# Performance work log

Hardware: AMD Instinct MI355X
Metric: run time of the kernel (lower is better)

## Reference

```python
import jax, jax.numpy as jnp
import numpy as np

HIDDEN_DIM = 1024
SEQ_LEN = 4096
D_IN = 1024


def setup_inputs() -> dict:
    key = jax.random.key(0)
    ks = jax.random.split(key, 9)
    s = 1.0 / np.sqrt(D_IN)
    return {
        "q": jax.random.normal(ks[0], (SEQ_LEN, D_IN), jnp.float32),
        "k": jax.random.normal(ks[1], (SEQ_LEN, D_IN), jnp.float32),
        "v": jax.random.normal(ks[2], (SEQ_LEN, D_IN), jnp.float32),
        "Wq": jax.random.normal(ks[3], (D_IN, HIDDEN_DIM), jnp.float32) * s,
        "bq": jnp.zeros((HIDDEN_DIM,), jnp.float32),
        "Wk": jax.random.normal(ks[4], (D_IN, HIDDEN_DIM), jnp.float32) * s,
        "bk": jnp.zeros((HIDDEN_DIM,), jnp.float32),
        "Wv": jax.random.normal(ks[5], (D_IN, HIDDEN_DIM), jnp.float32) * s,
        "bv": jnpp_zeros() if False else jnp.zeros((HIDDEN_DIM,), jnp.float32),
    }


def reference(q, k, v, Wq, bq, Wk, bk, Wv, bv):
    # Dense projections (flax Dense: x @ W + b)
    query = q @ Wq + bq          # [S, H]
    key_p = k @ Wk + bk          # [S, H]
    value = v @ Wv + bv          # [S, H]
    # scores = Q K^T / sqrt(hidden_dim)  -> [S, S]
    scores = jnp.matmul(query, key_p.T) / jnp.sqrt(jnp.float32(HIDDEN_DIM))
    weights = jax.nn.softmax(scores, axis=-1)
    context = jnp.matmul(weights, value)  # [S, H]
    return context
```

## Files before the change

### kernel.cpp

```cpp
#include <hip/hip_runtime.h>


typedef short short4v __attribute__((ext_vector_type(4)));
typedef short short8  __attribute__((ext_vector_type(8)));
typedef float f32x4   __attribute__((ext_vector_type(4)));

#define MFMA16 __builtin_amdgcn_mfma_f32_16x16x32_bf16

__device__ __forceinline__ short f2bf(float f) {
    union { float f; unsigned u; } x; x.f = f;
    unsigned r = (x.u + 0x7FFFu + ((x.u >> 16) & 1u)) >> 16;
    return (short)r;
}
__device__ __forceinline__ float bf2f(short s) {
    union { unsigned u; float f; } x;
    x.u = ((unsigned)(unsigned short)s) << 16; return x.f;
}
__device__ __forceinline__ void store_out(short* p, float v) { *p = f2bf(v); }
__device__ __forceinline__ void store_out(float* p, float v) { *p = v; }

__device__ __forceinline__ void gl2lds(const short* g, short* l) {
    __builtin_amdgcn_global_load_lds(
        (const __attribute__((address_space(1))) void*)g,
        (__attribute__((address_space(3))) void*)l, 16, 0, 0);
}

__global__ __launch_bounds__(256) void prep_w(
    const float* __restrict__ W0, const float* __restrict__ W1,
    const float* __restrict__ W2, short* __restrict__ Wt)
{
    __shared__ float tile[64][65];
    const float* W = blockIdx.z == 0 ? W0 : (blockIdx.z == 1 ? W1 : W2);
    short* T = Wt + (size_t)blockIdx.z * 1048576;
    const int c0 = blockIdx.x * 64;
    const int r0 = blockIdx.y * 64;
    const int tx = threadIdx.x & 63;
    const int ty = threadIdx.x >> 6;
    #pragma unroll
    for (int p = 0; p < 16; ++p) {
        int r = ty + p * 4;
        tile[r][tx] = W[(size_t)(r0 + r) * 1024 + c0 + tx];
    }
    __syncthreads();
    #pragma unroll
    for (int p = 0; p < 16; ++p) {
        int r = ty + p * 4;
        T[(size_t)(c0 + r) * 1024 + r0 + tx] = f2bf(tile[tx][r]);
    }
}

__global__ __launch_bounds__(256) void cast_qkv(
    const float* __restrict__ q, const float* __restrict__ k,
    const float* __restrict__ v, short* __restrict__ xb)
{
    const float* src = blockIdx.z == 0 ? q : (blockIdx.z == 1 ? k : v);
    short* dst = xb + (size_t)blockIdx.z * 4194304;
    for (int i = blockIdx.x * 256 + threadIdx.x; i < 1048576; i += 256 * 1024) {
        float4 f = ((const float4*)src)[i];
        short4v o;
        o[0] = f2bf(f.x); o[1] = f2bf(f.y); o[2] = f2bf(f.z); o[3] = f2bf(f.w);
        ((short4v*)dst)[i] = o;
    }
}

__global__ __launch_bounds__(256) void transpose_v(
    const short* __restrict__ src, short* __restrict__ dst)
{
    __shared__ short t[64][65];
    const int c0 = blockIdx.x * 64;
    const int r0 = blockIdx.y * 64;
    const int tx = threadIdx.x & 63;
    const int ty = threadIdx.x >> 6;
    #pragma unroll
    for (int p = 0; p < 16; ++p) {
        const int r = p * 4 + ty;
        t[r][tx] = src[(size_t)(r0 + r) * 1024 + c0 + tx];
    }
    __syncthreads();
    #pragma unroll
    for (int p = 0; p < 16; ++p) {
        const int r = p * 4 + ty;
        dst[(size_t)(c0 + r) * 4096 + r0 + tx] = t[tx][r];
    }
}

template <typename TOut, int MODE>
__global__ __launch_bounds__(512, 2) void gemm256(
    const short* __restrict__ A, const short* __restrict__ Bt,
    const float* __restrict__ b0, const float* __restrict__ b1,
    const float* __restrict__ b2,
    TOut* __restrict__ C, float* __restrict__ P1, float* __restrict__ P2,
    float* __restrict__ P3,
    int M, int N, int lda, int ldb, float scale,
    int nc, int nc_last, int kstep)
{
    __shared__ short Lds[65536];

    const int t    = threadIdx.x;
    const int lane = t & 63;
    const int wv   = t >> 6;

    int m0, n0;
    {
        const int nb  = gridDim.x;
        const int bid = blockIdx.y * nb + blockIdx.x;
        if (nb == 16 && gridDim.y == 16) {
            const int x = bid & 7, i = bid >> 3;
            m0 = ((x & 1) * 8 + (i & 7)) * 256;
            n0 = ((x >> 1) * 4 + (i >> 3)) * 256;
        } else {
            const int band   = bid / (8 * nb);
            const int within = bid - band * 8 * nb;
            m0 = (band * 8 + (within & 7)) * 256;
            n0 = (within >> 3) * 256;
        }
    }

    const float* bias = nullptr;
    int kbeg = 0;
    TOut* Cw = C;
    if constexpr (MODE == 1) {
        const int z = blockIdx.z;
        A  += (size_t)z * M * lda;
        Bt += (size_t)z * N * ldb;
        Cw  = C + (size_t)z * M * N;
        bias = z == 0 ? b0 : (z == 1 ? b1 : b2);
    }
    if constexpr (MODE == 2) {
        const int z = blockIdx.z;
        kbeg = z * kstep;
        if (z == (int)gridDim.z - 1) nc = nc_last;
        Cw = (TOut*)(z == 0 ? (float*)C : (z == 1 ? P1 : (z == 2 ? P2 : P3)));
    }
    (void)b0; (void)b1; (void)b2; (void)P1; (void)P2; (void)P3;
    (void)nc_last; (void)kstep;

    const int srow = lane >> 2;
    const int skof = ((lane & 3) ^ ((lane >> 3) & 3)) * 8;
    const short* pA0 = A  + (size_t)(m0 + wv * 16 + srow) * lda + kbeg + skof;
    const short* pA1 = pA0 + (size_t)128 * lda;
    const short* pB0 = Bt + (size_t)(n0 + wv * 16 + srow) * ldb + kbeg + skof;
    const short* pB1 = pB0 + (size_t)128 * ldb;
    short* sA0 = Lds + wv * 512;
    short* sA1 = Lds + 4096  + wv * 512;
    short* sB0 = Lds + 8192  + wv * 512;
    short* sB1 = Lds + 12288 + wv * 512;

    const int wm = wv >> 2, wn = wv & 3;
    const int lr = lane & 15, lq = lane >> 4;
    const int pcol = lq ^ ((lr >> 1) & 3);
    const short* rdA = Lds + (wm * 128 + lr) * 32 + pcol * 8;
    const short* rdB = Lds + 8192 + (wn * 64 + lr) * 32 + pcol * 8;

    f32x4 acc[8][4];
    #pragma unroll
    for (int i = 0; i < 8; ++i)
        #pragma unroll
        for (int j = 0; j < 4; ++j) { f32x4 z4 = {0.f,0.f,0.f,0.f}; acc[i][j] = z4; }

#define STAGE_A(c) {                                                      \
    const int su_ = (c) & 3;                                              \
    const size_t ko_ = (size_t)(c) * 32;                                  \
    gl2lds(pA0 + ko_, sA0 + su_ * 16384);                                 \
    gl2lds(pA1 + ko_, sA1 + su_ * 16384); }
#define STAGE_B(c) {                                                      \
    const int su_ = (c) & 3;                                              \
    const size_t ko_ = (size_t)(c) * 32;                                  \
    gl2lds(pB0 + ko_, sB0 + su_ * 16384);                                 \
    gl2lds(pB1 + ko_, sB1 + su_ * 16384); }

    STAGE_A(0); STAGE_B(0);
    STAGE_A(1); STAGE_B(1);
    STAGE_A(2); STAGE_B(2);
    asm volatile("s_waitcnt vmcnt(8)" ::: "memory");
    __builtin_amdgcn_s_barrier();

#define PHASE(c, DOSTAGE, VMN) {                                          \
    const int u_ = (c) & 3;                                               \
    const short* rA_ = rdA + u_ * 16384;                                  \
    const short* rB_ = rdB + u_ * 16384;                                  \
    short8 af[4], bfr[4];                                                 \
    _Pragma("unroll") for (int i = 0; i < 4; ++i)                         \
        af[i] = *(const short8*)(rA_ + i * 512);                          \
    _Pragma("unroll") for (int j = 0; j < 4; ++j)                         \
        bfr[j] = *(const short8*)(rB_ + j * 512);                         \
    if (DOSTAGE) STAGE_A((c) + 3);                                        \
    __builtin_amdgcn_s_barrier();                                         \
    __builtin_amdgcn_s_setprio(1);                                        \
    _Pragma("unroll") for (int i = 0; i < 4; ++i)                         \
        _Pragma("unroll") for (int j = 0; j < 4; ++j)                     \
            acc[i][j] = MFMA16(af[i], bfr[j], acc[i][j], 0, 0, 0);        \
    __builtin_amdgcn_s_setprio(0);                                        \
    __builtin_amdgcn_s_barrier();                                         \
    _Pragma("unroll") for (int i = 0; i < 4; ++i)                         \
        af[i] = *(const short8*)(rA_ + (4 + i) * 512);                    \
    if (DOSTAGE) STAGE_B((c) + 3);                                        \
    __builtin_amdgcn_s_barrier();                                         \
    __builtin_amdgcn_s_setprio(1);                                        \
    _Pragma("unroll") for (int i = 0; i < 4; ++i)                         \
        _Pragma("unroll") for (int j = 0; j < 4; ++j)                     \
            acc[4 + i][j] = MFMA16(af[i], bfr[j], acc[4 + i][j], 0, 0, 0);\
    __builtin_amdgcn_s_setprio(0);                                        \
    if ((VMN) == 8)      asm volatile("s_waitcnt vmcnt(8)" ::: "memory"); \
    else if ((VMN) == 4) asm volatile("s_waitcnt vmcnt(4)" ::: "memory"); \
    else if ((VMN) == 0) asm volatile("s_waitcnt vmcnt(0)" ::: "memory"); \
    if ((VMN) >= 0) __builtin_amdgcn_s_barrier(); }

    #pragma unroll 4
    for (int c = 0; c < nc - 3; ++c) PHASE(c, 1, 8);
    PHASE(nc - 3, 0, 4);
    PHASE(nc - 2, 0, 0);
    PHASE(nc - 1, 0, -1);
#undef PHASE
#undef STAGE_A
#undef STAGE_B

    #pragma unroll
    for (int i = 0; i < 8; ++i) {
        const int crow = m0 + wm * 128 + i * 16 + lq * 4;
        #pragma unroll
        for (int j = 0; j < 4; ++j) {
            const int ccol = n0 + wn * 64 + j * 16 + lr;
            float bb = 0.f;
            if constexpr (MODE == 1) bb = bias[ccol];
            #pragma unroll
            for (int r = 0; r < 4; ++r) {
                float val = acc[i][j][r] * scale + bb;
                store_out(&Cw[(size_t)(crow + r) * N + ccol], val);
            }
        }
    }
}

__global__ __launch_bounds__(256) void softmax_bf16(short* __restrict__ S)
{
    const int row = blockIdx.x;
    short8* r8 = (short8*)(S + (size_t)row * 4096);
    const int t = threadIdx.x;

    float x[16];
    #pragma unroll
    for (int i = 0; i < 2; ++i) {
        short8 raw = r8[t + 256 * i];
        #pragma unroll
        for (int j = 0; j < 8; ++j) x[8 * i + j] = bf2f(raw[j]);
    }
    float m = -1e30f;
    #pragma unroll
    for (int i = 0; i < 16; ++i) m = fmaxf(m, x[i]);
    #pragma unroll
    for (int off = 32; off > 0; off >>= 1) m = fmaxf(m, __shfl_xor(m, off));

    __shared__ float redm[4], reds[4];
    const int wv = t >> 6;
    if ((t & 63) == 0) redm[wv] = m;
    __syncthreads();
    m = fmaxf(fmaxf(redm[0], redm[1]), fmaxf(redm[2], redm[3]));

    float s = 0.f;
    #pragma unroll
    for (int i = 0; i < 16; ++i) { x[i] = __expf(x[i] - m); s += x[i]; }
    #pragma unroll
    for (int off = 32; off > 0; off >>= 1) s += __shfl_xor(s, off);
    if ((t & 63) == 0) reds[wv] = s;
    __syncthreads();
    s = reds[0] + reds[1] + reds[2] + reds[3];
    const float inv = 1.f / s;

    #pragma unroll
    for (int i = 0; i < 2; ++i) {
        short8 o;
        #pragma unroll
        for (int j = 0; j < 8; ++j) o[j] = f2bf(x[8 * i + j] * inv);
        r8[t + 256 * i] = o;
    }
}

__global__ __launch_bounds__(256) void combine(
    float* __restrict__ out, const float* __restrict__ a,
    const float* __restrict__ b, const float* __restrict__ c, int np)
{
    for (int i = blockIdx.x * 256 + threadIdx.x; i < 1048576; i += 256 * 1024) {
        float4 o = ((const float4*)out)[i];
        float4 x = ((const float4*)a)[i];
        float4 y = ((const float4*)b)[i];
        o.x += x.x + y.x; o.y += x.y + y.y;
        o.z += x.z + y.z; o.w += x.w + y.w;
        if (np == 3) {
            float4 w = ((const float4*)c)[i];
            o.x += w.x; o.y += w.y; o.z += w.z; o.w += w.w;
        }
        ((float4*)out)[i] = o;
    }
}

extern "C" void kernel_launch(void* const* d_in, const int* in_sizes, int n_in,
                              void* d_out, int out_size, void* d_ws, size_t ws_size,
                              hipStream_t stream)
{
    const float* q  = (const float*)d_in[0];
    const float* k  = (const float*)d_in[1];
    const float* v  = (const float*)d_in[2];
    const float* Wq = (const float*)d_in[3];
    const float* bq = (const float*)d_in[4];
    const float* Wk = (const float*)d_in[5];
    const float* bk = (const float*)d_in[6];
    const float* Wv = (const float*)d_in[7];
    const float* bv = (const float*)d_in[8];
    float* out = (float*)d_out;

    char* ws = (char*)d_ws;
    const size_t MB = 1ull << 20;
    short* Wt = (short*)(ws + 0);
    short* xb = (short*)(ws + 6 * MB);
    short* pr = (short*)(ws + 30 * MB);
    short* S  = (short*)(ws + 46 * MB);
    short* Vt = (short*)(ws + 78 * MB);
    float* p1 = (float*)(ws + 0);
    float* p2 = (float*)(ws + 16 * MB);
    float* p3 = (float*)(ws + 86 * MB);
    const int SK = (ws_size >= 102 * MB) ? 4 : 3;

    prep_w<<<dim3(16, 16, 3), 256, 0, stream>>>(Wq, Wk, Wv, Wt);
    cast_qkv<<<dim3(1024, 1, 3), 256, 0, stream>>>(q, k, v, xb);
    gemm256<short, 1><<<dim3(4, 16, 3), 512, 0, stream>>>(
        xb, Wt, bq, bk, bv, pr, nullptr, nullptr, nullptr,
        4096, 1024, 1024, 1024, 1.f, 32, 32, 0);
    transpose_v<<<dim3(16, 64), 256, 0, stream>>>(pr + 8 * 1024 * 1024, Vt);
    gemm256<short, 0><<<dim3(16, 16), 512, 0, stream>>>(
        pr, pr + 4 * 1024 * 1024, nullptr, nullptr, nullptr, S,
        nullptr, nullptr, nullptr,
        4096, 4096, 1024, 1024, 0.03125f, 32, 32, 0);
    softmax_bf16<<<4096, 256, 0, stream>>>(S);
    if (SK == 4) {
        gemm256<float, 2><<<dim3(4, 16, 4), 512, 0, stream>>>(
            S, Vt, nullptr, nullptr, nullptr, out, p1, p2, p3,
            4096, 1024, 4096, 4096, 1.f, 32, 32, 1024);
        combine<<<1024, 256, 0, stream>>>(out, p1, p2, p3, 3);
    } else {
        gemm256<float, 2><<<dim3(4, 16, 3), 512, 0, stream>>>(
            S, Vt, nullptr, nullptr, nullptr, out, p1, p2, nullptr,
            4096, 1024, 4096, 4096, 1.f, 42, 44, 1344);
        combine<<<1024, 256, 0, stream>>>(out, p1, p2, nullptr, 2);
    }
}
```

Measured before the change: 253.3 us.

## Process two K-chunks per pipeline step with quadrant-ordered MFMA scheduling

The main GEMM loop now handles two 32-wide K chunks per iteration, issuing the A and B prefetches for the next pair of chunks at two points. MFMAs are grouped by output quadrant, and B fragments are split so register pressure is spread across four barrier-separated phases. The prologue prefetches four chunks instead of three. The goal is fewer barriers and waitcnts per unit of K and better overlap of LDS loads with MFMA work. In exchange it uses more fragment registers, and the loop count assumes nc is even.

```diff
diff --git a/kernel.cpp b/kernel.cpp
--- a/kernel.cpp
+++ b/kernel.cpp
@@ -169,49 +169,86 @@
     gl2lds(pB0 + ko_, sB0 + su_ * 16384);                                 \
     gl2lds(pB1 + ko_, sB1 + su_ * 16384); }
 
-    STAGE_A(0); STAGE_B(0);
-    STAGE_A(1); STAGE_B(1);
-    STAGE_A(2); STAGE_B(2);
+    STAGE_A(0); STAGE_B(0); STAGE_A(1); STAGE_B(1);
+    STAGE_A(2); STAGE_B(2); STAGE_A(3); STAGE_B(3);
     asm volatile("s_waitcnt vmcnt(8)" ::: "memory");
     __builtin_amdgcn_s_barrier();
 
-#define PHASE(c, DOSTAGE, VMN) {                                          \
-    const int u_ = (c) & 3;                                               \
-    const short* rA_ = rdA + u_ * 16384;                                  \
-    const short* rB_ = rdB + u_ * 16384;                                  \
-    short8 af[4], bfr[4];                                                 \
-    _Pragma("unroll") for (int i = 0; i < 4; ++i)                         \
-        af[i] = *(const short8*)(rA_ + i * 512);                          \
-    _Pragma("unroll") for (int j = 0; j < 4; ++j)                         \
-        bfr[j] = *(const short8*)(rB_ + j * 512);                         \
-    if (DOSTAGE) STAGE_A((c) + 3);                                        \
+    const int nt = nc >> 1;
+
+#define TILE(t, DOSTAGE, VMN) {                                           \
+    const int u0_ = (2 * (t)) & 3;                                        \
+    const short* a0_ = rdA + u0_ * 16384;                                 \
+    const short* a1_ = a0_ + 16384;                                       \
+    const short* b0_ = rdB + u0_ * 16384;                                 \
+    const short* b1_ = b0_ + 16384;                                       \
+    short8 af[8], bfr[4], bg[4];                                          \
+          \
+    _Pragma("unroll") for (int mi = 0; mi < 4; ++mi) {                    \
+        af[mi * 2]     = *(const short8*)(a0_ + mi * 512);                \
+        af[mi * 2 + 1] = *(const short8*)(a1_ + mi * 512);                \
+    }                                                                     \
+    _Pragma("unroll") for (int nj = 0; nj < 2; ++nj) {                    \
+        bfr[nj * 2]     = *(const short8*)(b0_ + nj * 512);               \
+        bfr[nj * 2 + 1] = *(const short8*)(b1_ + nj * 512);               \
+    }                                                                     \
     __builtin_amdgcn_s_barrier();                                         \
     __builtin_amdgcn_s_setprio(1);                                        \
-    _Pragma("unroll") for (int i = 0; i < 4; ++i)                         \
-        _Pragma("unroll") for (int j = 0; j < 4; ++j)                     \
-            acc[i][j] = MFMA16(af[i], bfr[j], acc[i][j], 0, 0, 0);        \
+    _Pragma("unroll") for (int mi = 0; mi < 4; ++mi)                      \
+        _Pragma("unroll") for (int nj = 0; nj < 2; ++nj) {                \
+            acc[mi][nj] = MFMA16(af[mi*2],   bfr[nj*2],   acc[mi][nj], 0,0,0); \
+            acc[mi][nj] = MFMA16(af[mi*2+1], bfr[nj*2+1], acc[mi][nj], 0,0,0); \
+        }                                                                 \
     __builtin_amdgcn_s_setprio(0);                                        \
     __builtin_amdgcn_s_barrier();                                         \
-    _Pragma("unroll") for (int i = 0; i < 4; ++i)                         \
-        af[i] = *(const short8*)(rA_ + (4 + i) * 512);                    \
-    if (DOSTAGE) STAGE_B((c) + 3);                                        \
+      \
+    _Pragma("unroll") for (int nj = 0; nj < 2; ++nj) {                    \
+        bg[nj * 2]     = *(const short8*)(b0_ + (2 + nj) * 512);          \
+        bg[nj * 2 + 1] = *(const short8*)(b1_ + (2 + nj) * 512);          \
+    }                                                                     \
     __builtin_amdgcn_s_barrier();                                         \
     __builtin_amdgcn_s_setprio(1);                                        \
-    _Pragma("unroll") for (int i = 0; i < 4; ++i)                         \
-        _Pragma("unroll") for (int j = 0; j < 4; ++j)                     \
-            acc[4 + i][j] = MFMA16(af[i], bfr[j], acc[4 + i][j], 0, 0, 0);\
+    _Pragma("unroll") for (int mi = 0; mi < 4; ++mi)                      \
+        _Pragma("unroll") for (int nj = 0; nj < 2; ++nj) {                \
+            acc[mi][2+nj] = MFMA16(af[mi*2],   bg[nj*2],   acc[mi][2+nj], 0,0,0); \
+            acc[mi][2+nj] = MFMA16(af[mi*2+1], bg[nj*2+1], acc[mi][2+nj], 0,0,0); \
+        }                                                                 \
+    __builtin_amdgcn_s_setprio(0);                                        \
+    __builtin_amdgcn_s_barrier();                                         \
+            \
+    _Pragma("unroll") for (int mi = 0; mi < 4; ++mi) {                    \
+        af[mi * 2]     = *(const short8*)(a0_ + (4 + mi) * 512);          \
+        af[mi * 2 + 1] = *(const short8*)(a1_ + (4 + mi) * 512);          \
+    }                                                                     \
+    if (DOSTAGE) { STAGE_B(2 * (t) + 4); STAGE_B(2 * (t) + 5); }          \
+    __builtin_amdgcn_s_barrier();                                         \
+    __builtin_amdgcn_s_setprio(1);                                        \
+    _Pragma("unroll") for (int mi = 0; mi < 4; ++mi)                      \
+        _Pragma("unroll") for (int nj = 0; nj < 2; ++nj) {                \
+            acc[4+mi][nj] = MFMA16(af[mi*2],   bfr[nj*2],   acc[4+mi][nj], 0,0,0); \
+            acc[4+mi][nj] = MFMA16(af[mi*2+1], bfr[nj*2+1], acc[4+mi][nj], 0,0,0); \
+        }                                                                 \
+    __builtin_amdgcn_s_setprio(0);                                        \
+    __builtin_amdgcn_s_barrier();                                         \
+            \
+    if (DOSTAGE) { STAGE_A(2 * (t) + 4); STAGE_A(2 * (t) + 5); }          \
+    __builtin_amdgcn_s_barrier();                                         \
+    __builtin_amdgcn_s_setprio(1);                                        \
+    _Pragma("unroll") for (int mi = 0; mi < 4; ++mi)                      \
+        _Pragma("unroll") for (int nj = 0; nj < 2; ++nj) {                \
+            acc[4+mi][2+nj] = MFMA16(af[mi*2],   bg[nj*2],   acc[4+mi][2+nj], 0,0,0); \
+            acc[4+mi][2+nj] = MFMA16(af[mi*2+1], bg[nj*2+1], acc[4+mi][2+nj], 0,0,0); \
+        }                                                                 \
     __builtin_amdgcn_s_setprio(0);                                        \
     if ((VMN) == 8)      asm volatile("s_waitcnt vmcnt(8)" ::: "memory"); \
-    else if ((VMN) == 4) asm volatile("s_waitcnt vmcnt(4)" ::: "memory"); \
     else if ((VMN) == 0) asm volatile("s_waitcnt vmcnt(0)" ::: "memory"); \
     if ((VMN) >= 0) __builtin_amdgcn_s_barrier(); }
 
-    #pragma unroll 4
-    for (int c = 0; c < nc - 3; ++c) PHASE(c, 1, 8);
-    PHASE(nc - 3, 0, 4);
-    PHASE(nc - 2, 0, 0);
-    PHASE(nc - 1, 0, -1);
-#undef PHASE
+    #pragma unroll 2
+    for (int tt = 0; tt < nt - 2; ++tt) TILE(tt, 1, 8);
+    TILE(nt - 2, 0, 0);
+    TILE(nt - 1, 0, -1);
+#undef TILE
 #undef STAGE_A
 #undef STAGE_B
 
```

Result: no change. 254.6 us (+0.5%).
